# Optimization experiments

Measured on AMD Instinct MI355X. Metric: run time of the kernel, lower is better.

The kernel has to match this reference:

```python
import jax, jax.numpy as jnp
import numpy as np

N_NODES = 50000
N_EDGES = 800000
D_IN, D_HID, D_OUT = 128, 128, 64


def setup_inputs() -> dict:
    key = jax.random.key(0)
    ks = jax.random.split(key, 8)
    x = jax.random.normal(ks[0], (N_NODES, D_IN), dtype=jnp.float32)
    edge_index = jax.random.randint(ks[1], (2, N_EDGES), 0, N_NODES, dtype=jnp.int64)
    s1 = 1.0 / np.sqrt(D_IN)
    s2 = 1.0 / np.sqrt(D_HID)
    # PyG SAGEConv: out = lin_l(mean_aggr(x_j)) + lin_r(x_root); bias lives in lin_l
    Wl1 = jax.random.uniform(ks[2], (D_HID, D_IN), jnp.float32, -s1, s1)
    bl1 = jnp.zeros((D_HID,), jnp.float32)
    Wr1 = jax.random.uniform(ks[3], (D_HID, D_IN), jnp.float32, -s1, s1)
    Wl2 = jax.random.uniform(ks[4], (D_OUT, D_HID), jnp.float32, -s2, s2)
    bl2 = jnp.zeros((D_OUT,), jnp.float32)
    Wr2 = jax.random.uniform(ks[5], (D_OUT, D_HID), jnp.float32, -s2, s2)
    return {"x": x, "edge_index": edge_index, "Wl1": Wl1, "bl1": bl1, "Wr1": Wr1,
            "Wl2": Wl2, "bl2": bl2, "Wr2": Wr2}


def _sage_conv(x, src, dst, Wl, bl, Wr):
    # mean aggregation of source-node features onto destination nodes
    msg = x[src]                                              # [E, d]
    agg = jax.ops.segment_sum(msg, dst, num_segments=N_NODES)  # [N, d]
    cnt = jax.ops.segment_sum(jnp.ones((src.shape[0],), x.dtype), dst,
                              num_segments=N_NODES)            # [N]
    mean = agg / jnp.maximum(cnt, 1.0)[:, None]
    return mean @ Wl.T + bl + x @ Wr.T


def reference(x, edge_index, Wl1, bl1, Wr1, Wl2, bl2, Wr2):
    src, dst = edge_index[0], edge_index[1]
    h = jax.nn.relu(_sage_conv(x, src, dst, Wl1, bl1, Wr1))
    h = jax.nn.relu(_sage_conv(h, src, dst, Wl2, bl2, Wr2))
    return jax.nn.log_softmax(h, axis=-1)
```

## Files before the change

### kernel.cpp

```cpp
#include <hip/hip_runtime.h>
#include <cstdint>
#include <cstddef>

#define N_NODES 50000
#define N_EDGES 800000
#define ROWS_PAD 50048
#define ZROW 50000
#define BUCKET_CAP 64

typedef _Float16 f16;
typedef _Float16 f16x2 __attribute__((ext_vector_type(2)));
typedef _Float16 f16x8 __attribute__((ext_vector_type(8)));
typedef float f32x4 __attribute__((ext_vector_type(4)));
typedef unsigned short us4 __attribute__((ext_vector_type(4)));


#define EPT 16
#define CHUNK (256 * EPT)
#define NCHUNK ((N_EDGES + CHUNK - 1) / CHUNK)
#define NB_FILL (NCHUNK * 8)
#define NB_CX 12500
#define NB_CW 192
#define RANGE_SZ (N_NODES / 8)

__global__ __launch_bounds__(256) void preprocess_kernel(
    const int* __restrict__ edge, int* __restrict__ cnt, unsigned short* __restrict__ bucket,
    const float* __restrict__ x, f16* __restrict__ A1,
    const float* __restrict__ Wl1, const float* __restrict__ Wr1,
    const float* __restrict__ Wl2, const float* __restrict__ Wr2,
    f16* __restrict__ Wc1, f16* __restrict__ Wc2) {
  const int b = blockIdx.x;
  if (b < NB_FILL) {
    const int range = b & 7, chunk = b >> 3;
    const int lo = range * RANGE_SZ;
    const int hi = lo + RANGE_SZ;
    const int base = chunk * CHUNK + threadIdx.x;
    #pragma unroll
    for (int i = 0; i < EPT; ++i) {
      const int e = base + i * 256;
      if (e < N_EDGES) {
        const int dst = edge[N_EDGES + e];
        if (dst >= lo && dst < hi) {
          const int src = edge[e];
          const int pos = atomicAdd(&cnt[dst], 1);
          if (pos < BUCKET_CAP) bucket[(size_t)dst * BUCKET_CAP + pos] = (unsigned short)src;
        }
      }
    }
  } else if (b < NB_FILL + NB_CX) {
    const int idx = (b - NB_FILL) * 256 + threadIdx.x;
    const int row = idx >> 6, c2 = idx & 63;
    const float2 v = *reinterpret_cast<const float2*>(x + (size_t)row * 128 + c2 * 2);
    f16x2 o;
    o.x = (f16)v.x;
    o.y = (f16)v.y;
    *reinterpret_cast<f16x2*>(A1 + (size_t)row * 256 + 128 + c2 * 2) = o;
  } else if (b < NB_FILL + NB_CX + NB_CW) {
    const int idx = (b - NB_FILL - NB_CX) * 256 + threadIdx.x;
    if (idx < 128 * 256) {
      const int n = idx >> 8, k = idx & 255;
      const float v = (k < 128) ? Wl1[n * 128 + k] : Wr1[n * 128 + (k - 128)];
      Wc1[idx] = (f16)v;
    } else {
      const int j = idx - 128 * 256;
      const int n = j >> 8, k = j & 255;
      const float v = (k < 128) ? Wl2[n * 128 + k] : Wr2[n * 128 + (k - 128)];
      Wc2[j] = (f16)v;
    }
  } else {
    if (threadIdx.x < 64)
      reinterpret_cast<f16x2*>(A1 + (size_t)ZROW * 256 + 128)[threadIdx.x] =
          (f16x2){(f16)0.f, (f16)0.f};
  }
}


__global__ __launch_bounds__(256) void aggregate_mean_kernel(
    f16* A, const int* __restrict__ cnt, const unsigned short* __restrict__ bucket) {
  const int wid = threadIdx.x >> 6, lane = threadIdx.x & 63;
  const int quad = lane >> 4, l16 = lane & 15;
  const int nb = blockIdx.x * 16 + wid * 4;
  const int node = nb + quad;
  const int dv = (lane < 4) ? cnt[nb + lane] : 0;
  const int dq = __shfl(dv, quad, 64);
  const int dqc = min(dq, BUCKET_CAP);
  int md = max(max(__shfl(dv, 0, 64), __shfl(dv, 1, 64)),
               max(__shfl(dv, 2, 64), __shfl(dv, 3, 64)));
  md = min(md, BUCKET_CAP);
  const us4 b4 = *reinterpret_cast<const us4*>(bucket + (size_t)node * BUCKET_CAP + l16 * 4);
  float acc[8];
  #pragma unroll
  for (int c = 0; c < 8; ++c) acc[c] = 0.f;
  const f16* Asrc = A + 128 + l16 * 8;
  for (int j = 0; j < md; j += 8) {
    f16x8 v[8];
    #pragma unroll
    for (int k = 0; k < 8; ++k) {
      const int slot = j + k;
      const int idx = __shfl((int)b4[k & 3], quad * 16 + (slot >> 2), 64);
      const int row = (slot < dqc) ? idx : ZROW;
      v[k] = *reinterpret_cast<const f16x8*>(Asrc + (size_t)row * 256);
    }
    #pragma unroll
    for (int k = 0; k < 8; ++k) {
      #pragma unroll
      for (int c = 0; c < 8; ++c) acc[c] += (float)v[k][c];
    }
  }
  const float inv = 1.0f / (float)(dq > 0 ? dq : 1);
  f16x8 o;
  #pragma unroll
  for (int c = 0; c < 8; ++c) o[c] = (f16)(acc[c] * inv);
  *reinterpret_cast<f16x8*>(A + (size_t)node * 256 + l16 * 8) = o;
}


__global__ __launch_bounds__(256) void mfma_gemm1_kernel(
    const f16* __restrict__ A, const f16* __restrict__ Wc,
    const float* __restrict__ bias, f16* __restrict__ out) {
  constexpr int NT = 8;
  const int wid = threadIdx.x >> 6, lane = threadIdx.x & 63;
  const int quad = lane >> 4, l16 = lane & 15;
  const int row0 = blockIdx.x * 64 + wid * 16;
  if (blockIdx.x == 0 && threadIdx.x < 64)
    reinterpret_cast<f16x2*>(out + (size_t)ZROW * 256 + 128)[threadIdx.x] =
        (f16x2){(f16)0.f, (f16)0.f};
  f32x4 acc[NT];
  #pragma unroll
  for (int t = 0; t < NT; ++t) acc[t] = (f32x4){0.f, 0.f, 0.f, 0.f};
  const f16x8* Arow = reinterpret_cast<const f16x8*>(A + (size_t)(row0 + l16) * 256) + quad;
  const f16x8* Wb = reinterpret_cast<const f16x8*>(Wc) + quad;
  #pragma unroll
  for (int s = 0; s < 8; ++s) {
    const f16x8 a = Arow[s * 4];
    #pragma unroll
    for (int t = 0; t < NT; ++t) {
      const f16x8 b = Wb[(t * 16 + l16) * 32 + s * 4];
      acc[t] = __builtin_amdgcn_mfma_f32_16x16x32_f16(a, b, acc[t], 0, 0, 0);
    }
  }
  #pragma unroll
  for (int t = 0; t < NT; ++t) {
    const int col = t * 16 + l16;
    const float bv = bias[col];
    #pragma unroll
    for (int r = 0; r < 4; ++r) {
      const int row = row0 + quad * 4 + r;
      if (row < N_NODES)
        out[(size_t)row * 256 + 128 + col] = (f16)fmaxf(acc[t][r] + bv, 0.f);
    }
  }
}


__global__ __launch_bounds__(256) void mfma_gemm2_softmax_kernel(
    const f16* __restrict__ A, const f16* __restrict__ Wc,
    const float* __restrict__ bias, float* __restrict__ out) {
  constexpr int NT = 4;
  const int wid = threadIdx.x >> 6, lane = threadIdx.x & 63;
  const int quad = lane >> 4, l16 = lane & 15;
  const int row0 = blockIdx.x * 64 + wid * 16;
  f32x4 acc[NT];
  #pragma unroll
  for (int t = 0; t < NT; ++t) acc[t] = (f32x4){0.f, 0.f, 0.f, 0.f};
  const f16x8* Arow = reinterpret_cast<const f16x8*>(A + (size_t)(row0 + l16) * 256) + quad;
  const f16x8* Wb = reinterpret_cast<const f16x8*>(Wc) + quad;
  #pragma unroll
  for (int s = 0; s < 8; ++s) {
    const f16x8 a = Arow[s * 4];
    #pragma unroll
    for (int t = 0; t < NT; ++t) {
      const f16x8 b = Wb[(t * 16 + l16) * 32 + s * 4];
      acc[t] = __builtin_amdgcn_mfma_f32_16x16x32_f16(a, b, acc[t], 0, 0, 0);
    }
  }
  float bv[NT];
  #pragma unroll
  for (int t = 0; t < NT; ++t) bv[t] = bias[t * 16 + l16];
  #pragma unroll
  for (int r = 0; r < 4; ++r) {
    float v[NT];
    #pragma unroll
    for (int t = 0; t < NT; ++t) v[t] = fmaxf(acc[t][r] + bv[t], 0.f);
    float m = fmaxf(fmaxf(v[0], v[1]), fmaxf(v[2], v[3]));
    #pragma unroll
    for (int off = 1; off < 16; off <<= 1) m = fmaxf(m, __shfl_xor(m, off, 64));
    float s = __expf(v[0] - m) + __expf(v[1] - m) + __expf(v[2] - m) + __expf(v[3] - m);
    #pragma unroll
    for (int off = 1; off < 16; off <<= 1) s += __shfl_xor(s, off, 64);
    const float ls = m + __logf(s);
    const int row = row0 + quad * 4 + r;
    if (row < N_NODES) {
      #pragma unroll
      for (int t = 0; t < NT; ++t)
        out[(size_t)row * 64 + t * 16 + l16] = v[t] - ls;
    }
  }
}


extern "C" void kernel_launch(void* const* d_in, const int* in_sizes, int n_in,
                              void* d_out, int out_size, void* d_ws, size_t ws_size,
                              hipStream_t stream) {
  const float* x   = (const float*)d_in[0];
  const int* edge  = (const int*)d_in[1];
  const float* Wl1 = (const float*)d_in[2];
  const float* bl1 = (const float*)d_in[3];
  const float* Wr1 = (const float*)d_in[4];
  const float* Wl2 = (const float*)d_in[5];
  const float* bl2 = (const float*)d_in[6];
  const float* Wr2 = (const float*)d_in[7];
  float* out = (float*)d_out;

  char* ws = (char*)d_ws;
  size_t off = 0;
  auto alloc = [&](size_t bytes) -> char* {
    char* p = ws + off;
    off = (off + bytes + 255) & ~(size_t)255;
    return p;
  };
  int* cnt               = (int*)alloc((size_t)N_NODES * 4);
  unsigned short* bucket = (unsigned short*)alloc((size_t)N_NODES * BUCKET_CAP * 2);
  f16* A1 = (f16*)alloc((size_t)ROWS_PAD * 256 * 2);
  f16* A2 = (f16*)alloc((size_t)ROWS_PAD * 256 * 2);
  f16* Wc1 = (f16*)alloc((size_t)128 * 256 * 2);
  f16* Wc2 = (f16*)alloc((size_t)64 * 256 * 2);

  hipMemsetAsync(cnt, 0, (size_t)N_NODES * 4, stream);

  preprocess_kernel<<<NB_FILL + NB_CX + NB_CW + 1, 256, 0, stream>>>(
      edge, cnt, bucket, x, A1, Wl1, Wr1, Wl2, Wr2, Wc1, Wc2);

  aggregate_mean_kernel<<<N_NODES / 16, 256, 0, stream>>>(A1, cnt, bucket);
  mfma_gemm1_kernel<<<ROWS_PAD / 64, 256, 0, stream>>>(A1, Wc1, bl1, A2);

  aggregate_mean_kernel<<<N_NODES / 16, 256, 0, stream>>>(A2, cnt, bucket);
  mfma_gemm2_softmax_kernel<<<ROWS_PAD / 64, 256, 0, stream>>>(A2, Wc2, bl2, out);
}
```

Baseline: 235.2 us.

## Fuse mean aggregation into GEMM kernels via LDS and compact feature layout

Each layer's neighbor-mean aggregation now runs inside the GEMM kernel and writes its 64-row tile into shared memory, so the MFMA step reads the aggregated half from LDS and the root half from a compact 128-wide f16 feature array. This removes a kernel launch per layer and the round trip of the aggregated matrix through global memory. The gather stride is halved, which improves cache density, and the x conversion is vectorized to 8 halves per thread. Gathers are batched 16 deep instead of 8. The risk is higher register pressure and lower occupancy in the fused kernels, where the latency-bound gathers now share resources with the MFMA work.

```diff
diff --git a/kernel.cpp b/kernel.cpp
--- a/kernel.cpp
+++ b/kernel.cpp
@@ -19,22 +19,22 @@
 #define CHUNK (256 * EPT)
 #define NCHUNK ((N_EDGES + CHUNK - 1) / CHUNK)
 #define NB_FILL (NCHUNK * 8)
-#define NB_CX 12500
+#define NB_CX 3125
 #define NB_CW 192
 #define RANGE_SZ (N_NODES / 8)
 
 __global__ __launch_bounds__(256) void preprocess_kernel(
     const int* __restrict__ edge, int* __restrict__ cnt, unsigned short* __restrict__ bucket,
-    const float* __restrict__ x, f16* __restrict__ A1,
+    const float* __restrict__ x, f16* __restrict__ X16, f16* __restrict__ H16,
     const float* __restrict__ Wl1, const float* __restrict__ Wr1,
     const float* __restrict__ Wl2, const float* __restrict__ Wr2,
     f16* __restrict__ Wc1, f16* __restrict__ Wc2) {
   const int b = blockIdx.x;
+  const int tid = threadIdx.x;
   if (b < NB_FILL) {
-    const int range = b & 7, chunk = b >> 3;
-    const int lo = range * RANGE_SZ;
-    const int hi = lo + RANGE_SZ;
-    const int base = chunk * CHUNK + threadIdx.x;
+    const int r = b & 7, chunk = b >> 3;
+    const int lo = r * RANGE_SZ, hi = lo + RANGE_SZ;
+    const int base = chunk * CHUNK + tid;
     #pragma unroll
     for (int i = 0; i < EPT; ++i) {
       const int e = base + i * 256;
@@ -48,140 +48,151 @@
       }
     }
   } else if (b < NB_FILL + NB_CX) {
-    const int idx = (b - NB_FILL) * 256 + threadIdx.x;
-    const int row = idx >> 6, c2 = idx & 63;
-    const float2 v = *reinterpret_cast<const float2*>(x + (size_t)row * 128 + c2 * 2);
-    f16x2 o;
-    o.x = (f16)v.x;
-    o.y = (f16)v.y;
-    *reinterpret_cast<f16x2*>(A1 + (size_t)row * 256 + 128 + c2 * 2) = o;
+    const int idx = (b - NB_FILL) * 256 + tid;
+    const int row = idx >> 4, c8 = idx & 15;
+    const float4 v0 = *reinterpret_cast<const float4*>(x + (size_t)row * 128 + c8 * 8);
+    const float4 v1 = *reinterpret_cast<const float4*>(x + (size_t)row * 128 + c8 * 8 + 4);
+    f16x8 o;
+    o[0] = (f16)v0.x; o[1] = (f16)v0.y; o[2] = (f16)v0.z; o[3] = (f16)v0.w;
+    o[4] = (f16)v1.x; o[5] = (f16)v1.y; o[6] = (f16)v1.z; o[7] = (f16)v1.w;
+    *reinterpret_cast<f16x8*>(X16 + (size_t)row * 128 + c8 * 8) = o;
   } else if (b < NB_FILL + NB_CX + NB_CW) {
-    const int idx = (b - NB_FILL - NB_CX) * 256 + threadIdx.x;
+    const int idx = (b - NB_FILL - NB_CX) * 256 + tid;
     if (idx < 128 * 256) {
       const int n = idx >> 8, k = idx & 255;
-      const float v = (k < 128) ? Wl1[n * 128 + k] : Wr1[n * 128 + (k - 128)];
-      Wc1[idx] = (f16)v;
+      Wc1[idx] = (f16)((k < 128) ? Wl1[n * 128 + k] : Wr1[n * 128 + (k - 128)]);
     } else {
       const int j = idx - 128 * 256;
       const int n = j >> 8, k = j & 255;
-      const float v = (k < 128) ? Wl2[n * 128 + k] : Wr2[n * 128 + (k - 128)];
-      Wc2[j] = (f16)v;
+      Wc2[j] = (f16)((k < 128) ? Wl2[n * 128 + k] : Wr2[n * 128 + (k - 128)]);
     }
   } else {
-    if (threadIdx.x < 64)
-      reinterpret_cast<f16x2*>(A1 + (size_t)ZROW * 256 + 128)[threadIdx.x] =
-          (f16x2){(f16)0.f, (f16)0.f};
-  }
-}
-
-
-__global__ __launch_bounds__(256) void aggregate_mean_kernel(
-    f16* A, const int* __restrict__ cnt, const unsigned short* __restrict__ bucket) {
+    if (tid < 64)
+      reinterpret_cast<f16x2*>(X16 + (size_t)ZROW * 128)[tid] = (f16x2){(f16)0.f, (f16)0.f};
+    else if (tid < 128)
+      reinterpret_cast<f16x2*>(H16 + (size_t)ZROW * 128)[tid - 64] = (f16x2){(f16)0.f, (f16)0.f};
+  }
+}
+
+
+__device__ __forceinline__ void aggregate_to_lds(
+    const f16* __restrict__ F, const int* __restrict__ cnt,
+    const unsigned short* __restrict__ bucket,
+    f16 (*M)[136], int wid, int lane) {
+  const int quad = lane >> 4, l16 = lane & 15;
+  #pragma unroll 1
+  for (int g = 0; g < 4; ++g) {
+    const int nb = blockIdx.x * 64 + wid * 16 + g * 4;
+    const int node = nb + quad;
+    const int dv = (lane < 4) ? cnt[nb + lane] : 0;
+    const int dq = __shfl(dv, quad, 64);
+    const int dqc = min(dq, BUCKET_CAP);
+    int md = max(max(__shfl(dv, 0, 64), __shfl(dv, 1, 64)),
+                 max(__shfl(dv, 2, 64), __shfl(dv, 3, 64)));
+    md = min(md, BUCKET_CAP);
+    const us4 b4 = *reinterpret_cast<const us4*>(bucket + (size_t)node * BUCKET_CAP + l16 * 4);
+    float acc[8];
+    #pragma unroll
+    for (int c = 0; c < 8; ++c) acc[c] = 0.f;
+    const f16* Fsrc = F + l16 * 8;
+    for (int j = 0; j < md; j += 16) {
+      f16x8 v[16];
+      #pragma unroll
+      for (int k = 0; k < 16; ++k) {
+        const int slot = j + k;
+        const int idx = __shfl((int)b4[k & 3], quad * 16 + (slot >> 2), 64);
+        const int row = (slot < dqc) ? idx : ZROW;
+        v[k] = *reinterpret_cast<const f16x8*>(Fsrc + (size_t)row * 128);
+      }
+      #pragma unroll
+      for (int k = 0; k < 16; ++k) {
+        #pragma unroll
+        for (int c = 0; c < 8; ++c) acc[c] += (float)v[k][c];
+      }
+    }
+    const float inv = 1.0f / (float)(dq > 0 ? dq : 1);
+    f16x8 o;
+    #pragma unroll
+    for (int c = 0; c < 8; ++c) o[c] = (f16)(acc[c] * inv);
+    *reinterpret_cast<f16x8*>(&M[wid * 16 + g * 4 + quad][l16 * 8]) = o;
+  }
+}
+
+
+__global__ __launch_bounds__(256, 4) void layer1_kernel(
+    const f16* __restrict__ X16, const int* __restrict__ cnt,
+    const unsigned short* __restrict__ bucket, const f16* __restrict__ Wc,
+    const float* __restrict__ bias, f16* __restrict__ H16) {
+  __shared__ f16 M[64][136];
   const int wid = threadIdx.x >> 6, lane = threadIdx.x & 63;
   const int quad = lane >> 4, l16 = lane & 15;
-  const int nb = blockIdx.x * 16 + wid * 4;
-  const int node = nb + quad;
-  const int dv = (lane < 4) ? cnt[nb + lane] : 0;
-  const int dq = __shfl(dv, quad, 64);
-  const int dqc = min(dq, BUCKET_CAP);
-  int md = max(max(__shfl(dv, 0, 64), __shfl(dv, 1, 64)),
-               max(__shfl(dv, 2, 64), __shfl(dv, 3, 64)));
-  md = min(md, BUCKET_CAP);
-  const us4 b4 = *reinterpret_cast<const us4*>(bucket + (size_t)node * BUCKET_CAP + l16 * 4);
-  float acc[8];
-  #pragma unroll
-  for (int c = 0; c < 8; ++c) acc[c] = 0.f;
-  const f16* Asrc = A + 128 + l16 * 8;
-  for (int j = 0; j < md; j += 8) {
-    f16x8 v[8];
-    #pragma unroll
-    for (int k = 0; k < 8; ++k) {
-      const int slot = j + k;
-      const int idx = __shfl((int)b4[k & 3], quad * 16 + (slot >> 2), 64);
-      const int row = (slot < dqc) ? idx : ZROW;
-      v[k] = *reinterpret_cast<const f16x8*>(Asrc + (size_t)row * 256);
-    }
-    #pragma unroll
-    for (int k = 0; k < 8; ++k) {
-      #pragma unroll
-      for (int c = 0; c < 8; ++c) acc[c] += (float)v[k][c];
-    }
-  }
-  const float inv = 1.0f / (float)(dq > 0 ? dq : 1);
-  f16x8 o;
-  #pragma unroll
-  for (int c = 0; c < 8; ++c) o[c] = (f16)(acc[c] * inv);
-  *reinterpret_cast<f16x8*>(A + (size_t)node * 256 + l16 * 8) = o;
-}
-
-
-__global__ __launch_bounds__(256) void mfma_gemm1_kernel(
-    const f16* __restrict__ A, const f16* __restrict__ Wc,
-    const float* __restrict__ bias, f16* __restrict__ out) {
-  constexpr int NT = 8;
-  const int wid = threadIdx.x >> 6, lane = threadIdx.x & 63;
-  const int quad = lane >> 4, l16 = lane & 15;
+  aggregate_to_lds(X16, cnt, bucket, M, wid, lane);
+  __syncthreads();
   const int row0 = blockIdx.x * 64 + wid * 16;
-  if (blockIdx.x == 0 && threadIdx.x < 64)
-    reinterpret_cast<f16x2*>(out + (size_t)ZROW * 256 + 128)[threadIdx.x] =
-        (f16x2){(f16)0.f, (f16)0.f};
-  f32x4 acc[NT];
-  #pragma unroll
-  for (int t = 0; t < NT; ++t) acc[t] = (f32x4){0.f, 0.f, 0.f, 0.f};
-  const f16x8* Arow = reinterpret_cast<const f16x8*>(A + (size_t)(row0 + l16) * 256) + quad;
+  f32x4 acc[8];
+  #pragma unroll
+  for (int u = 0; u < 8; ++u) acc[u] = (f32x4){0.f, 0.f, 0.f, 0.f};
   const f16x8* Wb = reinterpret_cast<const f16x8*>(Wc) + quad;
+  const f16* Xrow = X16 + (size_t)(row0 + l16) * 128 + quad * 8;
   #pragma unroll
   for (int s = 0; s < 8; ++s) {
-    const f16x8 a = Arow[s * 4];
-    #pragma unroll
-    for (int t = 0; t < NT; ++t) {
-      const f16x8 b = Wb[(t * 16 + l16) * 32 + s * 4];
-      acc[t] = __builtin_amdgcn_mfma_f32_16x16x32_f16(a, b, acc[t], 0, 0, 0);
-    }
-  }
-  #pragma unroll
-  for (int t = 0; t < NT; ++t) {
-    const int col = t * 16 + l16;
+    const f16x8 a = (s < 4)
+        ? *reinterpret_cast<const f16x8*>(&M[wid * 16 + l16][quad * 8 + s * 32])
+        : *reinterpret_cast<const f16x8*>(Xrow + (s - 4) * 32);
+    #pragma unroll
+    for (int u = 0; u < 8; ++u) {
+      const f16x8 bb = Wb[(u * 16 + l16) * 32 + s * 4];
+      acc[u] = __builtin_amdgcn_mfma_f32_16x16x32_f16(a, bb, acc[u], 0, 0, 0);
+    }
+  }
+  #pragma unroll
+  for (int u = 0; u < 8; ++u) {
+    const int col = u * 16 + l16;
     const float bv = bias[col];
     #pragma unroll
     for (int r = 0; r < 4; ++r) {
       const int row = row0 + quad * 4 + r;
       if (row < N_NODES)
-        out[(size_t)row * 256 + 128 + col] = (f16)fmaxf(acc[t][r] + bv, 0.f);
-    }
-  }
-}
-
-
-__global__ __launch_bounds__(256) void mfma_gemm2_softmax_kernel(
-    const f16* __restrict__ A, const f16* __restrict__ Wc,
+        H16[(size_t)row * 128 + col] = (f16)fmaxf(acc[u][r] + bv, 0.f);
+    }
+  }
+}
+
+
+__global__ __launch_bounds__(256, 4) void layer2_kernel(
+    const f16* __restrict__ H16, const int* __restrict__ cnt,
+    const unsigned short* __restrict__ bucket, const f16* __restrict__ Wc,
     const float* __restrict__ bias, float* __restrict__ out) {
-  constexpr int NT = 4;
+  __shared__ f16 M[64][136];
   const int wid = threadIdx.x >> 6, lane = threadIdx.x & 63;
   const int quad = lane >> 4, l16 = lane & 15;
+  aggregate_to_lds(H16, cnt, bucket, M, wid, lane);
+  __syncthreads();
   const int row0 = blockIdx.x * 64 + wid * 16;
-  f32x4 acc[NT];
-  #pragma unroll
-  for (int t = 0; t < NT; ++t) acc[t] = (f32x4){0.f, 0.f, 0.f, 0.f};
-  const f16x8* Arow = reinterpret_cast<const f16x8*>(A + (size_t)(row0 + l16) * 256) + quad;
+  f32x4 acc[4];
+  #pragma unroll
+  for (int u = 0; u < 4; ++u) acc[u] = (f32x4){0.f, 0.f, 0.f, 0.f};
   const f16x8* Wb = reinterpret_cast<const f16x8*>(Wc) + quad;
+  const f16* Hrow = H16 + (size_t)(row0 + l16) * 128 + quad * 8;
   #pragma unroll
   for (int s = 0; s < 8; ++s) {
-    const f16x8 a = Arow[s * 4];
-    #pragma unroll
-    for (int t = 0; t < NT; ++t) {
-      const f16x8 b = Wb[(t * 16 + l16) * 32 + s * 4];
-      acc[t] = __builtin_amdgcn_mfma_f32_16x16x32_f16(a, b, acc[t], 0, 0, 0);
-    }
-  }
-  float bv[NT];
-  #pragma unroll
-  for (int t = 0; t < NT; ++t) bv[t] = bias[t * 16 + l16];
+    const f16x8 a = (s < 4)
+        ? *reinterpret_cast<const f16x8*>(&M[wid * 16 + l16][quad * 8 + s * 32])
+        : *reinterpret_cast<const f16x8*>(Hrow + (s - 4) * 32);
+    #pragma unroll
+    for (int u = 0; u < 4; ++u) {
+      const f16x8 bb = Wb[(u * 16 + l16) * 32 + s * 4];
+      acc[u] = __builtin_amdgcn_mfma_f32_16x16x32_f16(a, bb, acc[u], 0, 0, 0);
+    }
+  }
+  float bv[4];
+  #pragma unroll
+  for (int u = 0; u < 4; ++u) bv[u] = bias[u * 16 + l16];
   #pragma unroll
   for (int r = 0; r < 4; ++r) {
-    float v[NT];
-    #pragma unroll
-    for (int t = 0; t < NT; ++t) v[t] = fmaxf(acc[t][r] + bv[t], 0.f);
+    float v[4];
+    #pragma unroll
+    for (int u = 0; u < 4; ++u) v[u] = fmaxf(acc[u][r] + bv[u], 0.f);
     float m = fmaxf(fmaxf(v[0], v[1]), fmaxf(v[2], v[3]));
     #pragma unroll
     for (int off = 1; off < 16; off <<= 1) m = fmaxf(m, __shfl_xor(m, off, 64));
@@ -192,8 +203,8 @@
     const int row = row0 + quad * 4 + r;
     if (row < N_NODES) {
       #pragma unroll
-      for (int t = 0; t < NT; ++t)
-        out[(size_t)row * 64 + t * 16 + l16] = v[t] - ls;
+      for (int u = 0; u < 4; ++u)
+        out[(size_t)row * 64 + u * 16 + l16] = v[u] - ls;
     }
   }
 }
@@ -219,21 +230,18 @@
     off = (off + bytes + 255) & ~(size_t)255;
     return p;
   };
-  int* cnt               = (int*)alloc((size_t)N_NODES * 4);
-  unsigned short* bucket = (unsigned short*)alloc((size_t)N_NODES * BUCKET_CAP * 2);
-  f16* A1 = (f16*)alloc((size_t)ROWS_PAD * 256 * 2);
-  f16* A2 = (f16*)alloc((size_t)ROWS_PAD * 256 * 2);
+  int* cnt               = (int*)alloc((size_t)ROWS_PAD * 4);
+  unsigned short* bucket = (unsigned short*)alloc((size_t)ROWS_PAD * BUCKET_CAP * 2);
+  f16* X16 = (f16*)alloc((size_t)ROWS_PAD * 128 * 2);
+  f16* H16 = (f16*)alloc((size_t)ROWS_PAD * 128 * 2);
   f16* Wc1 = (f16*)alloc((size_t)128 * 256 * 2);
   f16* Wc2 = (f16*)alloc((size_t)64 * 256 * 2);
 
-  hipMemsetAsync(cnt, 0, (size_t)N_NODES * 4, stream);
+  hipMemsetAsync(cnt, 0, (size_t)ROWS_PAD * 4, stream);
 
   preprocess_kernel<<<NB_FILL + NB_CX + NB_CW + 1, 256, 0, stream>>>(
-      edge, cnt, bucket, x, A1, Wl1, Wr1, Wl2, Wr2, Wc1, Wc2);
-
-  aggregate_mean_kernel<<<N_NODES / 16, 256, 0, stream>>>(A1, cnt, bucket);
-  mfma_gemm1_kernel<<<ROWS_PAD / 64, 256, 0, stream>>>(A1, Wc1, bl1, A2);
-
-  aggregate_mean_kernel<<<N_NODES / 16, 256, 0, stream>>>(A2, cnt, bucket);
-  mfma_gemm2_softmax_kernel<<<ROWS_PAD / 64, 256, 0, stream>>>(A2, Wc2, bl2, out);
-}
+      edge, cnt, bucket, x, X16, H16, Wl1, Wr1, Wl2, Wr2, Wc1, Wc2);
+
+  layer1_kernel<<<ROWS_PAD / 64, 256, 0, stream>>>(X16, cnt, bucket, Wc1, bl1, H16);
+  layer2_kernel<<<ROWS_PAD / 64, 256, 0, stream>>>(H16, cnt, bucket, Wc2, bl2, out);
+}
```

Result: faster. 228.2 us (-3.0%).
